# Kernel tuning notes

Measured on AMD Instinct MI355X. Metric: run time of the kernel, lower is better.

## Reference

```python
import jax, jax.numpy as jnp
import numpy as np

B, C_IN, C_MID, C_OUT, H, W = 256, 2, 128, 64, 15, 15
N_RES = 4  # line_length//2 - 1 with line_length=11

# per-direction input offsets for kernel taps w0 and w2 (w1 is always center),
# matching fix_direction_order=True sparse 3x3 kernel construction:
# dir0 horizontal, dir1 vertical, dir2 anti-diagonal, dir3 main diagonal.
OFFSETS = (((0, -1), (0, 1)),
           ((-1, 0), (1, 0)),
           ((1, -1), (-1, 1)),
           ((-1, -1), (1, 1)))


def shift2d(x, di, dj):
    # out[..., i, j] = x[..., i+di, j+dj] with zero padding (di,dj in {-1,0,1})
    nd = x.ndim
    xp = jnp.pad(x, [(0, 0)] * (nd - 2) + [(1, 1), (1, 1)])
    h, w = x.shape[-2], x.shape[-1]
    return xp[..., 1 + di:1 + di + h, 1 + dj:1 + dj + w]


def dir_conv(x, w, b):
    # x: [4,B,Cin,H,W]; w: [Cout,Cin,3]; b: [Cout]
    x0 = jnp.stack([shift2d(x[d], *OFFSETS[d][0]) for d in range(4)])
    x2 = jnp.stack([shift2d(x[d], *OFFSETS[d][1]) for d in range(4)])
    y = (jnp.einsum('oc,dbchw->dbohw', w[..., 0], x0)
         + jnp.einsum('oc,dbchw->dbohw', w[..., 1], x)
         + jnp.einsum('oc,dbchw->dbohw', w[..., 2], x2))
    return y + b[None, None, :, None, None]


def conv1x1(x, w, b):
    # x: [4,B,Cin,H,W]; w: [Cout,Cin]; b: [Cout]
    return jnp.einsum('oc,dbchw->dbohw', w, x) + b[None, None, :, None, None]


def setup_inputs() -> dict:
    key = jax.random.key(0)
    ks = jax.random.split(key, 16)
    s_in = 1.0 / np.sqrt(3 * C_IN)
    s_mid = 1.0 / np.sqrt(3 * C_MID)
    s_pw = 1.0 / np.sqrt(C_MID)
    return {
        'x': jax.random.normal(ks[0], (B, C_IN, H, W), jnp.float32),
        'dconv0_w': jax.random.normal(ks[1], (C_MID, C_IN, 3), jnp.float32) * s_in,
        'dconv0_b': jnp.zeros((C_MID,), jnp.float32),
        'res_dconv_w': jax.random.normal(ks[2], (N_RES, C_MID, C_MID, 3), jnp.float32) * s_mid,
        'res_dconv_b': jnp.zeros((N_RES, C_MID), jnp.float32),
        'res_pw_w': jax.random.normal(ks[3], (N_RES, C_MID, C_MID), jnp.float32) * s_pw,
        'res_pw_b': jnp.zeros((N_RES, C_MID), jnp.float32),
        'c0_w1': jax.random.normal(ks[4], (C_MID, C_MID), jnp.float32) * s_pw,
        'c0_b1': jnp.zeros((C_MID,), jnp.float32),
        'c0_w2': jax.random.normal(ks[5], (C_MID, C_MID), jnp.float32) * s_pw,
        'c0_b2': jnp.zeros((C_MID,), jnp.float32),
        'final_w': jax.random.normal(ks[6], (C_OUT, C_MID), jnp.float32) * s_pw,
        'final_b': jnp.zeros((C_OUT,), jnp.float32),
    }


def reference(x, dconv0_w, dconv0_b, res_dconv_w, res_dconv_b,
              res_pw_w, res_pw_b, c0_w1, c0_b1, c0_w2, c0_b2,
              final_w, final_b):
    act = jax.nn.silu
    # all 4 direction streams start from the same input plane
    h = jnp.broadcast_to(x[None], (4,) + x.shape)  # [4,B,Cin,H,W]
    h = act(dir_conv(h, dconv0_w, dconv0_b))
    # DirectionalConvResBlocks (norm='none')
    for i in range(N_RES):
        r = h
        h = act(dir_conv(h, res_dconv_w[i], res_dconv_b[i]))
        h = act(conv1x1(h, res_pw_w[i], res_pw_b[i]))
        h = h + r
    # Conv0dResBlock (two 1x1 convs, middle_dim_multipler=1)
    r = h
    h = act(conv1x1(h, c0_w1, c0_b1))
    h = act(conv1x1(h, c0_w2, c0_b2))
    h = h + r
    # final 1x1 conv, then stack directions at dim=1 -> [B,4,Cout,H,W]
    h = conv1x1(h, final_w, final_b)
    return jnp.transpose(h, (1, 0, 2, 3, 4))
```

## Files before the change

kernel.cpp:

```cpp
#include <hip/hip_runtime.h>

using u16 = unsigned short;
using u32 = unsigned int;

typedef __bf16 bf16x8 __attribute__((ext_vector_type(8)));
typedef float  f32x4  __attribute__((ext_vector_type(4)));

#define NPOS   225
#define NT     15
#define ROWP   136
#define A_ROWS 289
#define A_ELEMS (A_ROWS*ROWP)
#define LDS_BYTES ((A_ELEMS + 1024)*2)
#define RSTRIDE17 (17*ROWP)

#define WA_PER_L 49152
#define WP_OFF   (4*WA_PER_L)
#define WP_PER   16384
#define WF_OFF   (WP_OFF + 6*WP_PER)
#define W_U16_TOTAL (WF_OFF + 8192)

__host__ __device__ __forceinline__ int permc(int c){
  return (c & ~0x3C) | (((c >> 2) & 3) << 4) | (((c >> 4) & 3) << 2);
}

__device__ __forceinline__ float bflo(u32 q){ return __uint_as_float(q << 16); }
__device__ __forceinline__ float bfhi(u32 q){ return __uint_as_float(q & 0xffff0000u); }
__device__ __forceinline__ u16 f2bf(float f){
  u32 u = __float_as_uint(f);
  return (u16)((u + 0x7fffu + ((u >> 16) & 1u)) >> 16);
}
__device__ __forceinline__ u32 packbf(float a, float b){
  union { __bf16 h[2]; u32 u; } r;
  r.h[0] = (__bf16)a; r.h[1] = (__bf16)b;
  return r.u;
}
__device__ __forceinline__ float silu_f(float x){
  return x * __builtin_amdgcn_rcpf(1.f + __expf(-x));
}
__device__ __forceinline__ f32x4 mfma16(bf16x8 a, bf16x8 b, f32x4 c){
  return __builtin_amdgcn_mfma_f32_16x16x32_bf16(a, b, c, 0, 0, 0);
}
__device__ __forceinline__ uint4 pack_silu2(const f32x4& a, const f32x4& b){
  uint4 q;
  q.x = packbf(silu_f(a[0]), silu_f(a[1]));
  q.y = packbf(silu_f(a[2]), silu_f(a[3]));
  q.z = packbf(silu_f(b[0]), silu_f(b[1]));
  q.w = packbf(silu_f(b[2]), silu_f(b[3]));
  return q;
}
__device__ __forceinline__ uint4 silu_add4(const f32x4& a, const f32x4& b, const uint4& r){
  uint4 q;
  q.x = packbf(silu_f(a[0]) + bflo(r.x), silu_f(a[1]) + bfhi(r.x));
  q.y = packbf(silu_f(a[2]) + bflo(r.y), silu_f(a[3]) + bfhi(r.y));
  q.z = packbf(silu_f(b[0]) + bflo(r.z), silu_f(b[1]) + bfhi(r.z));
  q.w = packbf(silu_f(b[2]) + bflo(r.w), silu_f(b[3]) + bfhi(r.w));
  return q;
}

__global__ void prep_w(const float* __restrict__ d0w, const float* __restrict__ d0b,
                       const float* __restrict__ rdw,
                       const float* __restrict__ rpw, const float* __restrict__ c1w,
                       const float* __restrict__ c2w, const float* __restrict__ fw,
                       float* __restrict__ ws)
{
  u16* wsb = (u16*)(ws + 896);
  const int total = 896 + W_U16_TOTAL;
  for (int idx = blockIdx.x*blockDim.x + threadIdx.x; idx < total; idx += gridDim.x*blockDim.x){
    if (idx < 768){
      int k = idx >> 7, s = idx & 127;
      ws[idx] = d0w[permc(s)*6 + k];
      continue;
    }
    if (idx < 896){
      int s = idx - 768;
      ws[idx] = d0b[permc(s)];
      continue;
    }
    int e = idx - 896;
    float v;
    if (e < WP_OFF){
      int L = e / WA_PER_L, r = e % WA_PER_L;
      int tap = r / 16384, r1 = r % 16384;
      int kb = r1 >> 12, ot = (r1 >> 9) & 7, l = (r1 >> 3) & 63, j = r1 & 7;
      int o = ot*16 + (l & 15);
      int ks = kb*32 + ((l >> 4) << 3) + j;
      v = rdw[((L*128 + o)*128 + permc(ks))*3 + tap];
    } else if (e < WF_OFF){
      int t2 = e - WP_OFF;
      int i = t2 / WP_PER, r = t2 % WP_PER;
      int kb = r >> 12, ot = (r >> 9) & 7, l = (r >> 3) & 63, j = r & 7;
      int o = ot*16 + (l & 15);
      int ks = kb*32 + ((l >> 4) << 3) + j;
      v = (i < 4) ? rpw[(i*128 + o)*128 + permc(ks)]
        : (i == 4) ? c1w[o*128 + permc(ks)] : c2w[o*128 + permc(ks)];
    } else {
      int e2 = e - WF_OFF;
      int kb = e2 >> 11, ot = (e2 >> 9) & 3, l = (e2 >> 3) & 63, j = e2 & 7;
      int o = ot*16 + (l & 15);
      int ks = kb*32 + ((l >> 4) << 3) + j;
      v = fw[o*128 + permc(ks)];
    }
    wsb[e] = f2bf(v);
  }
}

template<int NTL>
__device__ __forceinline__ void dconv_phase(f32x4 (&acc)[8][2],
    const u16* __restrict__ As, const u16* __restrict__ wd,
    const float* __restrict__ bd, int lane, int T0, int dr0, int dr2)
{
  const int col = lane & 15, kg = lane >> 4;
  #pragma unroll
  for (int ot=0; ot<8; ++ot){
    f32x4 bz = *(const f32x4*)(bd + ot*16 + kg*4);
    #pragma unroll
    for (int t=0;t<NTL;++t) acc[ot][t] = bz;
  }
  const int rb0 = ((T0+1)*17 + col + 1)*ROWP + kg*8;
  #pragma unroll 1
  for (int tap=0; tap<3; ++tap){
    const int offr = ((tap==0) ? dr0 : (tap==1) ? 0 : dr2)*ROWP;
    #pragma unroll 1
    for (int kb=0; kb<4; ++kb){
      bf16x8 w[8];
      #pragma unroll
      for (int ot=0; ot<8; ++ot)
        w[ot] = *(const bf16x8*)(wd + ((tap*4+kb)*8 + ot)*512 + lane*8);
      #pragma unroll
      for (int t=0; t<NTL; ++t){
        bf16x8 v = *(const bf16x8*)(As + rb0 + offr + t*RSTRIDE17 + kb*32);
        __builtin_amdgcn_s_setprio(1);
        acc[0][t] = mfma16(w[0], v, acc[0][t]);
        acc[1][t] = mfma16(w[1], v, acc[1][t]);
        acc[2][t] = mfma16(w[2], v, acc[2][t]);
        acc[3][t] = mfma16(w[3], v, acc[3][t]);
        acc[4][t] = mfma16(w[4], v, acc[4][t]);
        acc[5][t] = mfma16(w[5], v, acc[5][t]);
        acc[6][t] = mfma16(w[6], v, acc[6][t]);
        acc[7][t] = mfma16(w[7], v, acc[7][t]);
        __builtin_amdgcn_s_setprio(0);
      }
    }
  }
}

template<int NTL>
__device__ __forceinline__ void pwres_phase(f32x4 (&acc)[8][2],
    u16* __restrict__ As, const u16* __restrict__ wpw,
    const float* __restrict__ bp, int lane, int T0)
{
  const int col = lane & 15, kg = lane >> 4;
  const int rb0 = ((T0+1)*17 + col + 1)*ROWP;
  uint4 rsd[NTL][4];
  #pragma unroll
  for (int t=0;t<NTL;++t){
    const u16* rp = As + rb0 + t*RSTRIDE17 + kg*16;
    rsd[t][0] = *(const uint4*)rp;
    rsd[t][1] = *(const uint4*)(rp + 8);
    rsd[t][2] = *(const uint4*)(rp + 64);
    rsd[t][3] = *(const uint4*)(rp + 72);
  }
  #pragma unroll
  for (int t=0;t<NTL;++t){
    if (col < 15){
      u16* dp = As + rb0 + t*RSTRIDE17 + kg*16;
      *(uint4*)dp      = pack_silu2(acc[0][t], acc[1][t]);
      *(uint4*)(dp+8)  = pack_silu2(acc[2][t], acc[3][t]);
      *(uint4*)(dp+64) = pack_silu2(acc[4][t], acc[5][t]);
      *(uint4*)(dp+72) = pack_silu2(acc[6][t], acc[7][t]);
    }
  }
  #pragma unroll
  for (int t=0;t<NTL;++t){
    f32x4 a[8];
    #pragma unroll
    for (int ot=0;ot<8;++ot) a[ot] = *(const f32x4*)(bp + ot*16 + kg*4);
    const u16* srow = As + rb0 + t*RSTRIDE17 + kg*8;
    #pragma unroll 1
    for (int kb=0; kb<4; ++kb){
      bf16x8 w[8];
      #pragma unroll
      for (int ot=0; ot<8; ++ot)
        w[ot] = *(const bf16x8*)(wpw + (kb*8 + ot)*512 + lane*8);
      bf16x8 v = *(const bf16x8*)(srow + kb*32);
      __builtin_amdgcn_s_setprio(1);
      a[0] = mfma16(w[0], v, a[0]); a[1] = mfma16(w[1], v, a[1]);
      a[2] = mfma16(w[2], v, a[2]); a[3] = mfma16(w[3], v, a[3]);
      a[4] = mfma16(w[4], v, a[4]); a[5] = mfma16(w[5], v, a[5]);
      a[6] = mfma16(w[6], v, a[6]); a[7] = mfma16(w[7], v, a[7]);
      __builtin_amdgcn_s_setprio(0);
    }
    if (col < 15){
      u16* dp = As + rb0 + t*RSTRIDE17 + kg*16;
      *(uint4*)dp      = silu_add4(a[0], a[1], rsd[t][0]);
      *(uint4*)(dp+8)  = silu_add4(a[2], a[3], rsd[t][1]);
      *(uint4*)(dp+64) = silu_add4(a[4], a[5], rsd[t][2]);
      *(uint4*)(dp+72) = silu_add4(a[6], a[7], rsd[t][3]);
    }
  }
}

template<int NTL>
__device__ __forceinline__ void tail_phase(u16* __restrict__ As,
    const u16* __restrict__ w1, const u16* __restrict__ w2, const u16* __restrict__ wf,
    const float* __restrict__ b1, const float* __restrict__ b2, const float* __restrict__ bf,
    float* __restrict__ out, int lane, int T0, int bd)
{
  const int col = lane & 15, kg = lane >> 4;
  const int rb0 = ((T0+1)*17 + col + 1)*ROWP;
  uint4 rsd[NTL][4];
  #pragma unroll
  for (int t=0;t<NTL;++t){
    const u16* rp = As + rb0 + t*RSTRIDE17 + kg*16;
    rsd[t][0] = *(const uint4*)rp;
    rsd[t][1] = *(const uint4*)(rp + 8);
    rsd[t][2] = *(const uint4*)(rp + 64);
    rsd[t][3] = *(const uint4*)(rp + 72);
  }
  #pragma unroll
  for (int t=0;t<NTL;++t){
    f32x4 a[8];
    #pragma unroll
    for (int ot=0;ot<8;++ot) a[ot] = *(const f32x4*)(b1 + ot*16 + kg*4);
    const u16* srow = As + rb0 + t*RSTRIDE17 + kg*8;
    #pragma unroll 1
    for (int kb=0; kb<4; ++kb){
      bf16x8 w[8];
      #pragma unroll
      for (int ot=0; ot<8; ++ot)
        w[ot] = *(const bf16x8*)(w1 + (kb*8 + ot)*512 + lane*8);
      bf16x8 v = *(const bf16x8*)(srow + kb*32);
      __builtin_amdgcn_s_setprio(1);
      a[0] = mfma16(w[0], v, a[0]); a[1] = mfma16(w[1], v, a[1]);
      a[2] = mfma16(w[2], v, a[2]); a[3] = mfma16(w[3], v, a[3]);
      a[4] = mfma16(w[4], v, a[4]); a[5] = mfma16(w[5], v, a[5]);
      a[6] = mfma16(w[6], v, a[6]); a[7] = mfma16(w[7], v, a[7]);
      __builtin_amdgcn_s_setprio(0);
    }
    if (col < 15){
      u16* dp = As + rb0 + t*RSTRIDE17 + kg*16;
      *(uint4*)dp      = pack_silu2(a[0], a[1]);
      *(uint4*)(dp+8)  = pack_silu2(a[2], a[3]);
      *(uint4*)(dp+64) = pack_silu2(a[4], a[5]);
      *(uint4*)(dp+72) = pack_silu2(a[6], a[7]);
    }
  }
  #pragma unroll
  for (int t=0;t<NTL;++t){
    f32x4 a[8];
    #pragma unroll
    for (int ot=0;ot<8;++ot) a[ot] = *(const f32x4*)(b2 + ot*16 + kg*4);
    const u16* srow = As + rb0 + t*RSTRIDE17 + kg*8;
    #pragma unroll 1
    for (int kb=0; kb<4; ++kb){
      bf16x8 w[8];
      #pragma unroll
      for (int ot=0; ot<8; ++ot)
        w[ot] = *(const bf16x8*)(w2 + (kb*8 + ot)*512 + lane*8);
      bf16x8 v = *(const bf16x8*)(srow + kb*32);
      __builtin_amdgcn_s_setprio(1);
      a[0] = mfma16(w[0], v, a[0]); a[1] = mfma16(w[1], v, a[1]);
      a[2] = mfma16(w[2], v, a[2]); a[3] = mfma16(w[3], v, a[3]);
      a[4] = mfma16(w[4], v, a[4]); a[5] = mfma16(w[5], v, a[5]);
      a[6] = mfma16(w[6], v, a[6]); a[7] = mfma16(w[7], v, a[7]);
      __builtin_amdgcn_s_setprio(0);
    }
    if (col < 15){
      u16* dp = As + rb0 + t*RSTRIDE17 + kg*16;
      *(uint4*)dp      = silu_add4(a[0], a[1], rsd[t][0]);
      *(uint4*)(dp+8)  = silu_add4(a[2], a[3], rsd[t][1]);
      *(uint4*)(dp+64) = silu_add4(a[4], a[5], rsd[t][2]);
      *(uint4*)(dp+72) = silu_add4(a[6], a[7], rsd[t][3]);
    }
  }
  #pragma unroll
  for (int t=0;t<NTL;++t){
    f32x4 a4[4];
    #pragma unroll
    for (int ot=0;ot<4;++ot) a4[ot] = *(const f32x4*)(bf + ot*16 + kg*4);
    const u16* srow = As + rb0 + t*RSTRIDE17 + kg*8;
    #pragma unroll 1
    for (int kb=0; kb<4; ++kb){
      bf16x8 w[4];
      #pragma unroll
      for (int ot=0; ot<4; ++ot)
        w[ot] = *(const bf16x8*)(wf + (kb*4 + ot)*512 + lane*8);
      bf16x8 v = *(const bf16x8*)(srow + kb*32);
      __builtin_amdgcn_s_setprio(1);
      a4[0] = mfma16(w[0], v, a4[0]); a4[1] = mfma16(w[1], v, a4[1]);
      a4[2] = mfma16(w[2], v, a4[2]); a4[3] = mfma16(w[3], v, a4[3]);
      __builtin_amdgcn_s_setprio(0);
    }
    if (col < 15){
      #pragma unroll
      for (int ot=0; ot<4; ++ot){
        float* op = out + ((size_t)(bd*64 + ot*16 + kg*4))*NPOS + (T0+t)*15 + col;
        op[0]      = a4[ot][0];
        op[NPOS]   = a4[ot][1];
        op[2*NPOS] = a4[ot][2];
        op[3*NPOS] = a4[ot][3];
      }
    }
  }
}

__global__ void __launch_bounds__(512, 2)
mix9_main(const float* __restrict__ x,
          const float* __restrict__ b_rd,
          const float* __restrict__ b_rp,
          const float* __restrict__ b_c1,
          const float* __restrict__ b_c2,
          const float* __restrict__ b_fin,
          const float* __restrict__ wt,
          float* __restrict__ out)
{
  extern __shared__ u16 sm[];
  u16* As = sm;

  const int blk  = blockIdx.x;
  const int b    = blk >> 2, d = blk & 3;
  const int tid  = threadIdx.x;
  const int wave = __builtin_amdgcn_readfirstlane(tid >> 6);
  const int lane = tid & 63;
  const int T0   = 2*wave;

  const int DI0[4] = {0,-1, 1,-1}, DJ0[4] = {-1, 0,-1,-1};
  const int DI2[4] = {0, 1,-1, 1}, DJ2[4] = { 1, 0, 1, 1};
  const int di0 = DI0[d], dj0 = DJ0[d], di2 = DI2[d], dj2 = DJ2[d];
  const int dr0 = di0*17 + dj0;
  const int dr2 = di2*17 + dj2;

  for (int k2 = tid; k2 < A_ELEMS; k2 += 512) As[k2] = 0;
  float* xs = (float*)(As + A_ELEMS);
  if (tid < 450) xs[tid] = x[b*450 + tid];
  __syncthreads();

  {
    const float* b0p = wt + 768;
    const int ob = wave * 16;
    #pragma unroll 1
    for (int pb = 0; pb < 4; ++pb){
      int pp = pb*64 + lane;
      int i = pp >> 4, j = pp & 15;
      if (i >= 15 || j >= 15) continue;
      float acc0[16];
      #pragma unroll
      for (int oo=0;oo<16;++oo) acc0[oo] = b0p[ob+oo];
      #pragma unroll
      for (int c=0;c<2;++c){
        int i0=i+di0, j0=j+dj0, i2=i+di2, j2=j+dj2;
        float x0 = ((unsigned)i0<15u && (unsigned)j0<15u) ? xs[c*NPOS + i0*15 + j0] : 0.f;
        float x1 = xs[c*NPOS + i*15 + j];
        float x2 = ((unsigned)i2<15u && (unsigned)j2<15u) ? xs[c*NPOS + i2*15 + j2] : 0.f;
        const float* w0r = wt + (c*3+0)*128 + ob;
        const float* w1r = wt + (c*3+1)*128 + ob;
        const float* w2r = wt + (c*3+2)*128 + ob;
        #pragma unroll
        for (int oo=0;oo<16;++oo)
          acc0[oo] = fmaf(w0r[oo],x0, fmaf(w1r[oo],x1, fmaf(w2r[oo],x2, acc0[oo])));
      }
      u16* dp = As + ((i+1)*17 + (j+1))*ROWP + ob;
      #pragma unroll
      for (int oo=0;oo<16;oo+=2)
        *(u32*)(dp+oo) = packbf(silu_f(acc0[oo]), silu_f(acc0[oo+1]));
    }
  }
  __syncthreads();

  const u16* wsb = (const u16*)(wt + 896);
  f32x4 acc[8][2];

  #pragma unroll 1
  for (int L = 0; L < 4; ++L){
    if (wave < 7) dconv_phase<2>(acc, As, wsb + L*WA_PER_L, b_rd + L*128, lane, T0, dr0, dr2);
    else          dconv_phase<1>(acc, As, wsb + L*WA_PER_L, b_rd + L*128, lane, 14, dr0, dr2);
    __syncthreads();
    if (wave < 7) pwres_phase<2>(acc, As, wsb + WP_OFF + L*WP_PER, b_rp + L*128, lane, T0);
    else          pwres_phase<1>(acc, As, wsb + WP_OFF + L*WP_PER, b_rp + L*128, lane, 14);
    if (L < 3) __syncthreads();
  }

  if (wave < 7)
    tail_phase<2>(As, wsb + WP_OFF + 4*WP_PER, wsb + WP_OFF + 5*WP_PER, wsb + WF_OFF,
                  b_c1, b_c2, b_fin, out, lane, T0, b*4 + d);
  else
    tail_phase<1>(As, wsb + WP_OFF + 4*WP_PER, wsb + WP_OFF + 5*WP_PER, wsb + WF_OFF,
                  b_c1, b_c2, b_fin, out, lane, 14, b*4 + d);
}

extern "C" void kernel_launch(void* const* d_in, const int* in_sizes, int n_in,
                              void* d_out, int out_size, void* d_ws, size_t ws_size,
                              hipStream_t stream)
{
  const float* x     = (const float*)d_in[0];
  const float* w_d0  = (const float*)d_in[1];
  const float* b_d0  = (const float*)d_in[2];
  const float* w_rd  = (const float*)d_in[3];
  const float* b_rd  = (const float*)d_in[4];
  const float* w_rp  = (const float*)d_in[5];
  const float* b_rp  = (const float*)d_in[6];
  const float* w_c1  = (const float*)d_in[7];
  const float* b_c1  = (const float*)d_in[8];
  const float* w_c2  = (const float*)d_in[9];
  const float* b_c2  = (const float*)d_in[10];
  const float* w_fin = (const float*)d_in[11];
  const float* b_fin = (const float*)d_in[12];
  float* wt  = (float*)d_ws;
  float* out = (float*)d_out;

  prep_w<<<128, 512, 0, stream>>>(w_d0, b_d0, w_rd, w_rp, w_c1, w_c2, w_fin, wt);

  (void)hipFuncSetAttribute((const void*)mix9_main,
                            hipFuncAttributeMaxDynamicSharedMemorySize, LDS_BYTES);
  mix9_main<<<1024, 512, LDS_BYTES, stream>>>(x, b_rd, b_rp, b_c1, b_c2, b_fin, wt, out);
}
```

Baseline: 285.9 us.

## Shrink LDS tile to 16-wide rows with row guards, raise launch bounds

```diff
diff --git a/kernel.cpp b/kernel.cpp
--- a/kernel.cpp
+++ b/kernel.cpp
@@ -7,12 +7,11 @@
 typedef float  f32x4  __attribute__((ext_vector_type(4)));
 
 #define NPOS   225
-#define NT     15
 #define ROWP   136
-#define A_ROWS 289
-#define A_ELEMS (A_ROWS*ROWP)
-#define LDS_BYTES ((A_ELEMS + 1024)*2)
-#define RSTRIDE17 (17*ROWP)
+#define NROWS  240
+#define A_ELEMS (NROWS*ROWP)
+#define LDS_BYTES (A_ELEMS*2)
+#define RST16 (16*ROWP)
 
 #define WA_PER_L 49152
 #define WP_OFF   (4*WA_PER_L)
@@ -108,7 +107,8 @@
 template<int NTL>
 __device__ __forceinline__ void dconv_phase(f32x4 (&acc)[8][2],
     const u16* __restrict__ As, const u16* __restrict__ wd,
-    const float* __restrict__ bd, int lane, int T0, int dr0, int dr2)
+    const float* __restrict__ bd, int lane, int T0,
+    int dr0, int dr2, int di0, int di2)
 {
   const int col = lane & 15, kg = lane >> 4;
   #pragma unroll
@@ -117,10 +117,11 @@
     #pragma unroll
     for (int t=0;t<NTL;++t) acc[ot][t] = bz;
   }
-  const int rb0 = ((T0+1)*17 + col + 1)*ROWP + kg*8;
+  const int rb0 = (T0*16 + col)*ROWP + kg*8;
   #pragma unroll 1
   for (int tap=0; tap<3; ++tap){
-    const int offr = ((tap==0) ? dr0 : (tap==1) ? 0 : dr2)*ROWP;
+    const int di    = (tap==0) ? di0 : (tap==1) ? 0 : di2;
+    const int droff = ((tap==0) ? dr0 : (tap==1) ? 0 : dr2)*ROWP;
     #pragma unroll 1
     for (int kb=0; kb<4; ++kb){
       bf16x8 w[8];
@@ -129,17 +130,19 @@
         w[ot] = *(const bf16x8*)(wd + ((tap*4+kb)*8 + ot)*512 + lane*8);
       #pragma unroll
       for (int t=0; t<NTL; ++t){
-        bf16x8 v = *(const bf16x8*)(As + rb0 + offr + t*RSTRIDE17 + kb*32);
-        __builtin_amdgcn_s_setprio(1);
-        acc[0][t] = mfma16(w[0], v, acc[0][t]);
-        acc[1][t] = mfma16(w[1], v, acc[1][t]);
-        acc[2][t] = mfma16(w[2], v, acc[2][t]);
-        acc[3][t] = mfma16(w[3], v, acc[3][t]);
-        acc[4][t] = mfma16(w[4], v, acc[4][t]);
-        acc[5][t] = mfma16(w[5], v, acc[5][t]);
-        acc[6][t] = mfma16(w[6], v, acc[6][t]);
-        acc[7][t] = mfma16(w[7], v, acc[7][t]);
-        __builtin_amdgcn_s_setprio(0);
+        if ((unsigned)(T0 + t + di) < 15u){
+          bf16x8 v = *(const bf16x8*)(As + rb0 + t*RST16 + droff + kb*32);
+          __builtin_amdgcn_s_setprio(1);
+          acc[0][t] = mfma16(w[0], v, acc[0][t]);
+          acc[1][t] = mfma16(w[1], v, acc[1][t]);
+          acc[2][t] = mfma16(w[2], v, acc[2][t]);
+          acc[3][t] = mfma16(w[3], v, acc[3][t]);
+          acc[4][t] = mfma16(w[4], v, acc[4][t]);
+          acc[5][t] = mfma16(w[5], v, acc[5][t]);
+          acc[6][t] = mfma16(w[6], v, acc[6][t]);
+          acc[7][t] = mfma16(w[7], v, acc[7][t]);
+          __builtin_amdgcn_s_setprio(0);
+        }
       }
     }
   }
@@ -151,11 +154,11 @@
     const float* __restrict__ bp, int lane, int T0)
 {
   const int col = lane & 15, kg = lane >> 4;
-  const int rb0 = ((T0+1)*17 + col + 1)*ROWP;
+  const int rb0 = (T0*16 + col)*ROWP;
   uint4 rsd[NTL][4];
   #pragma unroll
   for (int t=0;t<NTL;++t){
-    const u16* rp = As + rb0 + t*RSTRIDE17 + kg*16;
+    const u16* rp = As + rb0 + t*RST16 + kg*16;
     rsd[t][0] = *(const uint4*)rp;
     rsd[t][1] = *(const uint4*)(rp + 8);
     rsd[t][2] = *(const uint4*)(rp + 64);
@@ -164,7 +167,7 @@
   #pragma unroll
   for (int t=0;t<NTL;++t){
     if (col < 15){
-      u16* dp = As + rb0 + t*RSTRIDE17 + kg*16;
+      u16* dp = As + rb0 + t*RST16 + kg*16;
       *(uint4*)dp      = pack_silu2(acc[0][t], acc[1][t]);
       *(uint4*)(dp+8)  = pack_silu2(acc[2][t], acc[3][t]);
       *(uint4*)(dp+64) = pack_silu2(acc[4][t], acc[5][t]);
@@ -176,7 +179,7 @@
     f32x4 a[8];
     #pragma unroll
     for (int ot=0;ot<8;++ot) a[ot] = *(const f32x4*)(bp + ot*16 + kg*4);
-    const u16* srow = As + rb0 + t*RSTRIDE17 + kg*8;
+    const u16* srow = As + rb0 + t*RST16 + kg*8;
     #pragma unroll 1
     for (int kb=0; kb<4; ++kb){
       bf16x8 w[8];
@@ -192,7 +195,7 @@
       __builtin_amdgcn_s_setprio(0);
     }
     if (col < 15){
-      u16* dp = As + rb0 + t*RSTRIDE17 + kg*16;
+      u16* dp = As + rb0 + t*RST16 + kg*16;
       *(uint4*)dp      = silu_add4(a[0], a[1], rsd[t][0]);
       *(uint4*)(dp+8)  = silu_add4(a[2], a[3], rsd[t][1]);
       *(uint4*)(dp+64) = silu_add4(a[4], a[5], rsd[t][2]);
@@ -208,11 +211,11 @@
     float* __restrict__ out, int lane, int T0, int bd)
 {
   const int col = lane & 15, kg = lane >> 4;
-  const int rb0 = ((T0+1)*17 + col + 1)*ROWP;
+  const int rb0 = (T0*16 + col)*ROWP;
   uint4 rsd[NTL][4];
   #pragma unroll
   for (int t=0;t<NTL;++t){
-    const u16* rp = As + rb0 + t*RSTRIDE17 + kg*16;
+    const u16* rp = As + rb0 + t*RST16 + kg*16;
     rsd[t][0] = *(const uint4*)rp;
     rsd[t][1] = *(const uint4*)(rp + 8);
     rsd[t][2] = *(const uint4*)(rp + 64);
@@ -223,7 +226,7 @@
     f32x4 a[8];
     #pragma unroll
     for (int ot=0;ot<8;++ot) a[ot] = *(const f32x4*)(b1 + ot*16 + kg*4);
-    const u16* srow = As + rb0 + t*RSTRIDE17 + kg*8;
+    const u16* srow = As + rb0 + t*RST16 + kg*8;
     #pragma unroll 1
     for (int kb=0; kb<4; ++kb){
       bf16x8 w[8];
@@ -239,7 +242,7 @@
       __builtin_amdgcn_s_setprio(0);
     }
     if (col < 15){
-      u16* dp = As + rb0 + t*RSTRIDE17 + kg*16;
+      u16* dp = As + rb0 + t*RST16 + kg*16;
       *(uint4*)dp      = pack_silu2(a[0], a[1]);
       *(uint4*)(dp+8)  = pack_silu2(a[2], a[3]);
       *(uint4*)(dp+64) = pack_silu2(a[4], a[5]);
@@ -251,7 +254,7 @@
     f32x4 a[8];
     #pragma unroll
     for (int ot=0;ot<8;++ot) a[ot] = *(const f32x4*)(b2 + ot*16 + kg*4);
-    const u16* srow = As + rb0 + t*RSTRIDE17 + kg*8;
+    const u16* srow = As + rb0 + t*RST16 + kg*8;
     #pragma unroll 1
     for (int kb=0; kb<4; ++kb){
       bf16x8 w[8];
@@ -267,7 +270,7 @@
       __builtin_amdgcn_s_setprio(0);
     }
     if (col < 15){
-      u16* dp = As + rb0 + t*RSTRIDE17 + kg*16;
+      u16* dp = As + rb0 + t*RST16 + kg*16;
       *(uint4*)dp      = silu_add4(a[0], a[1], rsd[t][0]);
       *(uint4*)(dp+8)  = silu_add4(a[2], a[3], rsd[t][1]);
       *(uint4*)(dp+64) = silu_add4(a[4], a[5], rsd[t][2]);
@@ -279,7 +282,7 @@
     f32x4 a4[4];
     #pragma unroll
     for (int ot=0;ot<4;++ot) a4[ot] = *(const f32x4*)(bf + ot*16 + kg*4);
-    const u16* srow = As + rb0 + t*RSTRIDE17 + kg*8;
+    const u16* srow = As + rb0 + t*RST16 + kg*8;
     #pragma unroll 1
     for (int kb=0; kb<4; ++kb){
       bf16x8 w[4];
@@ -305,7 +308,7 @@
   }
 }
 
-__global__ void __launch_bounds__(512, 2)
+__global__ void __launch_bounds__(512, 4)
 mix9_main(const float* __restrict__ x,
           const float* __restrict__ b_rd,
           const float* __restrict__ b_rp,
@@ -328,17 +331,16 @@
   const int DI0[4] = {0,-1, 1,-1}, DJ0[4] = {-1, 0,-1,-1};
   const int DI2[4] = {0, 1,-1, 1}, DJ2[4] = { 1, 0, 1, 1};
   const int di0 = DI0[d], dj0 = DJ0[d], di2 = DI2[d], dj2 = DJ2[d];
-  const int dr0 = di0*17 + dj0;
-  const int dr2 = di2*17 + dj2;
+  const int dr0 = di0*16 + dj0;
+  const int dr2 = di2*16 + dj2;
 
   for (int k2 = tid; k2 < A_ELEMS; k2 += 512) As[k2] = 0;
-  float* xs = (float*)(As + A_ELEMS);
-  if (tid < 450) xs[tid] = x[b*450 + tid];
   __syncthreads();
 
   {
     const float* b0p = wt + 768;
     const int ob = wave * 16;
+    const float* xb = x + b*450;
     #pragma unroll 1
     for (int pb = 0; pb < 4; ++pb){
       int pp = pb*64 + lane;
@@ -347,12 +349,14 @@
       float acc0[16];
       #pragma unroll
       for (int oo=0;oo<16;++oo) acc0[oo] = b0p[ob+oo];
+      int i0=i+di0, j0=j+dj0, i2=i+di2, j2=j+dj2;
+      bool v0 = ((unsigned)i0<15u) && ((unsigned)j0<15u);
+      bool v2 = ((unsigned)i2<15u) && ((unsigned)j2<15u);
       #pragma unroll
       for (int c=0;c<2;++c){
-        int i0=i+di0, j0=j+dj0, i2=i+di2, j2=j+dj2;
-        float x0 = ((unsigned)i0<15u && (unsigned)j0<15u) ? xs[c*NPOS + i0*15 + j0] : 0.f;
-        float x1 = xs[c*NPOS + i*15 + j];
-        float x2 = ((unsigned)i2<15u && (unsigned)j2<15u) ? xs[c*NPOS + i2*15 + j2] : 0.f;
+        float x0 = v0 ? xb[c*NPOS + i0*15 + j0] : 0.f;
+        float x1 = xb[c*NPOS + i*15 + j];
+        float x2 = v2 ? xb[c*NPOS + i2*15 + j2] : 0.f;
         const float* w0r = wt + (c*3+0)*128 + ob;
         const float* w1r = wt + (c*3+1)*128 + ob;
         const float* w2r = wt + (c*3+2)*128 + ob;
@@ -360,7 +364,7 @@
         for (int oo=0;oo<16;++oo)
           acc0[oo] = fmaf(w0r[oo],x0, fmaf(w1r[oo],x1, fmaf(w2r[oo],x2, acc0[oo])));
       }
-      u16* dp = As + ((i+1)*17 + (j+1))*ROWP + ob;
+      u16* dp = As + pp*ROWP + ob;
       #pragma unroll
       for (int oo=0;oo<16;oo+=2)
         *(u32*)(dp+oo) = packbf(silu_f(acc0[oo]), silu_f(acc0[oo+1]));
@@ -373,8 +377,8 @@
 
   #pragma unroll 1
   for (int L = 0; L < 4; ++L){
-    if (wave < 7) dconv_phase<2>(acc, As, wsb + L*WA_PER_L, b_rd + L*128, lane, T0, dr0, dr2);
-    else          dconv_phase<1>(acc, As, wsb + L*WA_PER_L, b_rd + L*128, lane, 14, dr0, dr2);
+    if (wave < 7) dconv_phase<2>(acc, As, wsb + L*WA_PER_L, b_rd + L*128, lane, T0, dr0, dr2, di0, di2);
+    else          dconv_phase<1>(acc, As, wsb + L*WA_PER_L, b_rd + L*128, lane, 14, dr0, dr2, di0, di2);
     __syncthreads();
     if (wave < 7) pwres_phase<2>(acc, As, wsb + WP_OFF + L*WP_PER, b_rp + L*128, lane, T0);
     else          pwres_phase<1>(acc, As, wsb + WP_OFF + L*WP_PER, b_rp + L*128, lane, 14);
@@ -411,7 +415,5 @@
 
   prep_w<<<128, 512, 0, stream>>>(w_d0, b_d0, w_rd, w_rp, w_c1, w_c2, w_fin, wt);
 
-  (void)hipFuncSetAttribute((const void*)mix9_main,
-                            hipFuncAttributeMaxDynamicSharedMemorySize, LDS_BYTES);
   mix9_main<<<1024, 512, LDS_BYTES, stream>>>(x, b_rd, b_rp, b_c1, b_c2, b_fin, wt, out);
 }
```

Result: slower. 503.1 us (+76.0%).
